# Performance work log

Measured on AMD Instinct MI355X. Metric: run time of the kernel, lower is better.

Reference implementation:

```python
import jax, jax.numpy as jnp
import numpy as np

B, N, D = 32, 2048, 320

def _init(key, shape, fan_in):
    return jax.random.normal(key, shape, dtype=jnp.float32) / np.sqrt(fan_in).astype(np.float32)

def setup_inputs() -> dict:
    key = jax.random.key(0)
    ks = jax.random.split(key, 11)
    return {
        "x": jax.random.normal(ks[0], (B, N, D), dtype=jnp.float32),
        # downs MLP: 320->160->80
        "W1": _init(ks[1], (320, 160), 320), "b1": jnp.zeros((160,), jnp.float32),
        "W2": _init(ks[2], (160, 80), 160),  "b2": jnp.zeros((80,), jnp.float32),
        # GraphConv1d layers: 80->40, 40->5
        "Wg1": _init(ks[3], (80, 40), 80),   "bg1": jnp.zeros((40,), jnp.float32),
        "Wg2": _init(ks[4], (40, 5), 40),    "bg2": jnp.zeros((5,), jnp.float32),
        # final classifier: 5->2
        "Wf": _init(ks[5], (5, 2), 5),       "bf": jnp.zeros((2,), jnp.float32),
    }

def _euclidean_adj(h):
    # h: [B, N, C] -> row-softmax of negative squared pairwise Euclidean distance [B, N, N]
    sq = jnp.sum(h * h, axis=-1, keepdims=True)               # [B, N, 1]
    d2 = sq - 2.0 * jnp.einsum('bnc,bmc->bnm', h, h) + jnp.swapaxes(sq, -1, -2)
    return jax.nn.softmax(-d2, axis=-1)

def _graph_conv(h, W, b):
    a = _euclidean_adj(h)                                     # dynamic adjacency
    agg = jnp.einsum('bnm,bmc->bnc', a, h)                    # neighbor aggregation
    return jax.nn.relu(agg @ W + b)

def reference(x, W1, b1, W2, b2, Wg1, bg1, Wg2, bg2, Wf, bf):
    h = jax.nn.relu(x @ W1 + b1)          # [B, N, 160]
    h = jax.nn.relu(h @ W2 + b2)          # [B, N, 80]
    h = _graph_conv(h, Wg1, bg1)          # [B, N, 40]
    h = _graph_conv(h, Wg2, bg2)          # [B, N, 5]
    h = jnp.mean(h, axis=1)               # Mean() over nodes -> [B, 5]
    logits = h @ Wf + bf                  # [B, 2]
    return jax.nn.softmax(logits, axis=-1)
```

## Files before the change

kernel.cpp:

```cpp
#include <hip/hip_runtime.h>
#include <math.h>

#define BB 32
#define NN 2048
#define D_IN 320
#define H1 160
#define H2 80
#define H4 5

typedef __attribute__((ext_vector_type(8))) short short8;
typedef __attribute__((ext_vector_type(4))) short short4v;
typedef __attribute__((ext_vector_type(4))) float f32x4;
typedef __attribute__((ext_vector_type(16))) float f32x16;

__device__ inline ushort f2bf(float f) {
    union { float f; unsigned u; } v; v.f = f;
    unsigned r = v.u + 0x7fff + ((v.u >> 16) & 1);
    return (ushort)(r >> 16);
}
__device__ inline float bf2f(ushort u) {
    union { float f; unsigned u; } v; v.u = ((unsigned)u) << 16;
    return v.f;
}
__device__ inline unsigned pkbf(float hi, float lo) {
    union { float f; unsigned u; } a, b; a.f = hi; b.f = lo;
    return __builtin_amdgcn_perm(a.u + 0x8000u, b.u + 0x8000u, 0x07060302u);
}
__device__ inline float fexp2(float x) {
    float r;
    asm("v_exp_f32 %0, %1" : "=v"(r) : "v"(x));
    return r;
}
union U2S { unsigned u[2]; short4v s; };
union U4S { unsigned u[4]; short8 s; short4v h[2]; };

#define LOG2E  1.44269504088896340736f
#define TWOL2E 2.88539008177792681472f

__global__ __launch_bounds__(256) void prep_weights_kernel(
    const float* __restrict__ W1, const float* __restrict__ W2,
    const float* __restrict__ Wg1, const float* __restrict__ bg1,
    const float* __restrict__ Wg2, const float* __restrict__ bg2,
    ushort* __restrict__ Wt1, ushort* __restrict__ Wt2,
    ushort* __restrict__ Wg1B, float* __restrict__ bg1P,
    ushort* __restrict__ Wg2A, float* __restrict__ bg2P)
{
    const int id0 = blockIdx.x * 256 + threadIdx.x;
    const int stride = gridDim.x * 256;
    for (int i = id0; i < H1 * D_IN; i += stride) {
        const int j = i / D_IN, c = i % D_IN;
        Wt1[i] = f2bf(W1[c * H1 + j]);
    }
    for (int i = id0; i < H2 * H1; i += stride) {
        const int j = i / H1, c = i % H1;
        Wt2[i] = f2bf(W2[c * H2 + j]);
    }
    for (int i = id0; i < 48 * 96; i += stride) {
        const int j = i / 96, c = i % 96;
        Wg1B[i] = (j < 40 && c < 80) ? f2bf(Wg1[c * 40 + j]) : (ushort)0;
    }
    for (int i = id0; i < 32 * 48; i += stride) {
        const int j = i / 48, c = i % 48;
        const int c4 = c & 15;
        const int pos = (c & ~15) + (c4 & 3) + (((c4 >> 3) & 1) << 2) + (((c4 >> 2) & 1) << 3);
        Wg2A[j * 48 + pos] = (j < 5 && c < 40) ? f2bf(Wg2[c * 5 + j]) : (ushort)0;
    }
    if (id0 < 64) bg1P[id0] = (id0 < 40) ? bg1[id0] : 0.f;
    if (id0 < 32) bg2P[id0] = (id0 < 5) ? bg2[id0] : 0.f;
}

__global__ __launch_bounds__(256) void mlp_mfma_kernel(
    const float* __restrict__ x,
    const ushort* __restrict__ Wt1, const float* __restrict__ b1,
    const ushort* __restrict__ Wt2, const float* __restrict__ b2,
    const ushort* __restrict__ Wg1B,
    ushort* __restrict__ h2, ushort* __restrict__ V1T, float* __restrict__ sq2)
{
    constexpr int XST  = 72;
    constexpr int W1ST = 72;
    constexpr int H1ST = 168;
    constexpr int RST  = 104;

    __shared__ __attribute__((aligned(16))) ushort h1t[64 * H1ST];
    __shared__ __attribute__((aligned(16))) ushort ws1[H1 * W1ST];
    __shared__ float b1s[H1];
    __shared__ float b2s[H2];

    ushort* xs = h1t;

    const int t = threadIdx.x;
    const int lane = t & 63, w = t >> 6;
    const int colid = lane & 15, quad = lane >> 4;
    const int i = blockIdx.x;
    const int b = ((i & 7) << 2) + ((i >> 3) & 3);
    const int n0 = (i >> 5) * 64;
    const int row0 = b * NN + n0;

    if (t < H1) b1s[t] = b1[t];
    if (t < H2) b2s[t] = b2[t];

    f32x4 c1[10];
    #pragma unroll
    for (int ns = 0; ns < 10; ++ns) c1[ns] = (f32x4){0.f, 0.f, 0.f, 0.f};

    float4 xr[4];
    short8 wr[5];
    {
        #pragma unroll
        for (int i2 = 0; i2 < 4; ++i2) {
            const int id = t + i2 * 256, row = id >> 4, c4 = id & 15;
            xr[i2] = *(const float4*)&x[(size_t)(row0 + row) * D_IN + c4 * 4];
        }
        #pragma unroll
        for (int i2 = 0; i2 < 5; ++i2) {
            const int id = t + i2 * 256, j = id >> 3, part = id & 7;
            wr[i2] = *(const short8*)&Wt1[j * D_IN + part * 8];
        }
    }

    for (int kc = 0; kc < 5; ++kc) {
        if (kc) __syncthreads();
        #pragma unroll
        for (int i2 = 0; i2 < 4; ++i2) {
            const int id = t + i2 * 256, row = id >> 4, c4 = id & 15;
            uint2 up;
            up.x = pkbf(xr[i2].y, xr[i2].x);
            up.y = pkbf(xr[i2].w, xr[i2].z);
            *(uint2*)&xs[row * XST + c4 * 4] = up;
        }
        #pragma unroll
        for (int i2 = 0; i2 < 5; ++i2) {
            const int id = t + i2 * 256, j = id >> 3, part = id & 7;
            *(short8*)&ws1[j * W1ST + part * 8] = wr[i2];
        }
        __syncthreads();
        if (kc < 4) {
            const int k0 = (kc + 1) * 64;
            #pragma unroll
            for (int i2 = 0; i2 < 4; ++i2) {
                const int id = t + i2 * 256, row = id >> 4, c4 = id & 15;
                xr[i2] = *(const float4*)&x[(size_t)(row0 + row) * D_IN + k0 + c4 * 4];
            }
            #pragma unroll
            for (int i2 = 0; i2 < 5; ++i2) {
                const int id = t + i2 * 256, j = id >> 3, part = id & 7;
                wr[i2] = *(const short8*)&Wt1[j * D_IN + k0 + part * 8];
            }
        }

        short8 af[2];
        #pragma unroll
        for (int kf = 0; kf < 2; ++kf)
            af[kf] = *(const short8*)&xs[(w * 16 + colid) * XST + kf * 32 + quad * 8];
        #pragma unroll
        for (int ns = 0; ns < 10; ++ns) {
            #pragma unroll
            for (int kf = 0; kf < 2; ++kf) {
                const short8 bf = *(const short8*)&ws1[(ns * 16 + colid) * W1ST + kf * 32 + quad * 8];
                c1[ns] = __builtin_amdgcn_mfma_f32_16x16x32_bf16(af[kf], bf, c1[ns], 0, 0, 0);
            }
        }
    }
    __syncthreads();

    #pragma unroll
    for (int ns = 0; ns < 10; ++ns) {
        const float bj = b1s[ns * 16 + colid];
        #pragma unroll
        for (int r = 0; r < 4; ++r)
            h1t[(w * 16 + quad * 4 + r) * H1ST + ns * 16 + colid] =
                f2bf(fmaxf(c1[ns][r] + bj, 0.f));
    }
    __asm__ volatile("s_waitcnt lgkmcnt(0)" ::: "memory");

    short8 a2[5];
    #pragma unroll
    for (int kf = 0; kf < 5; ++kf)
        a2[kf] = *(const short8*)&h1t[(w * 16 + colid) * H1ST + kf * 32 + quad * 8];

    f32x4 c2[5];
    #pragma unroll
    for (int js = 0; js < 5; ++js) {
        f32x4 acc = (f32x4){0.f, 0.f, 0.f, 0.f};
        #pragma unroll
        for (int kf = 0; kf < 5; ++kf) {
            const short8 wb = *(const short8*)&Wt2[(js * 16 + colid) * H1 + kf * 32 + quad * 8];
            acc = __builtin_amdgcn_mfma_f32_16x16x32_bf16(a2[kf], wb, acc, 0, 0, 0);
        }
        c2[js] = acc;
    }
    __syncthreads();

    ushort* h2row = h1t;
    float rsq[4] = {0.f, 0.f, 0.f, 0.f};
    #pragma unroll
    for (int js = 0; js < 5; ++js) {
        const float bj = b2s[js * 16 + colid];
        #pragma unroll
        for (int r = 0; r < 4; ++r) {
            const ushort u = f2bf(fmaxf(c2[js][r] + bj, 0.f));
            const float vv = bf2f(u);
            rsq[r] += vv * vv;
            h2[(size_t)(row0 + w * 16 + quad * 4 + r) * 80 + js * 16 + colid] = u;
            h2row[(w * 16 + quad * 4 + r) * RST + js * 16 + colid] = u;
        }
    }
    {
        const int zr = t >> 2, zc = t & 3;
        *(short4v*)&h2row[zr * RST + 80 + zc * 4] = (short4v){0, 0, 0, 0};
    }
    __asm__ volatile("s_waitcnt lgkmcnt(0)" ::: "memory");

    short8 a3[3];
    #pragma unroll
    for (int kf = 0; kf < 3; ++kf)
        a3[kf] = *(const short8*)&h2row[(w * 16 + colid) * RST + kf * 32 + quad * 8];

    f32x4 c3[3];
    #pragma unroll
    for (int js = 0; js < 3; ++js) {
        f32x4 acc = (f32x4){0.f, 0.f, 0.f, 0.f};
        #pragma unroll
        for (int kf = 0; kf < 3; ++kf) {
            const short8 wb = *(const short8*)&Wg1B[(js * 16 + colid) * 96 + kf * 32 + quad * 8];
            acc = __builtin_amdgcn_mfma_f32_16x16x32_bf16(a3[kf], wb, acc, 0, 0, 0);
        }
        c3[js] = acc;
    }

    #pragma unroll
    for (int m = 1; m <= 8; m <<= 1)
        #pragma unroll
        for (int r = 0; r < 4; ++r) rsq[r] += __shfl_xor(rsq[r], m);
    if (colid == 0) {
        #pragma unroll
        for (int r = 0; r < 4; ++r)
            sq2[(size_t)row0 + w * 16 + quad * 4 + r] = rsq[r] * LOG2E;
    }

    ushort* Tbuf = ws1;
    #pragma unroll
    for (int js = 0; js < 3; ++js)
        #pragma unroll
        for (int r = 0; r < 4; ++r)
            Tbuf[(js * 16 + colid) * 72 + w * 16 + quad * 4 + r] = f2bf(c3[js][r]);
    __syncthreads();
    const short8 ones8 = {16256, 16256, 16256, 16256, 16256, 16256, 16256, 16256};
    for (int id = t; id < 48 * 8; id += 256) {
        const int row = id >> 3, part = id & 7;
        const short8 val = (row == 40) ? ones8 : *(const short8*)&Tbuf[row * 72 + part * 8];
        *(short8*)&V1T[((size_t)b * 48 + row) * NN + n0 + part * 8] = val;
    }
}

template<int CK, int CV, int CVS, int ONES_CH, bool HAS_OUT, bool DO_MEAN, int C_OUT>
__global__ __launch_bounds__(256, 2) void attn_conv_kernel(
    const ushort* __restrict__ h, const ushort* __restrict__ hT,
    const float* __restrict__ sqg,
    const ushort* __restrict__ WtP, const float* __restrict__ biasP,
    ushort* __restrict__ ho, ushort* __restrict__ hoT, float* __restrict__ sqo,
    float* __restrict__ mean_out)
{
    constexpr int CF   = CK / 16;
    constexpr int CSV  = CV / 32;
    constexpr int KST  = CK + 8;
    constexpr int VST  = 64 + 8;
    constexpr int KPR  = CK / 8;
    constexpr int KTOT = 64 * KPR;
    constexpr int NK   = (KTOT + 255) / 256;
    constexpr int NV   = (CV * 8) / 256;
    constexpr int TST  = 136;
    constexpr int CS1  = ONES_CH / 32;
    constexpr int R1   = ((ONES_CH % 32) / 8) * 4 + (ONES_CH & 3);
    constexpr int BUFN = 64 * KST + CV * VST;

    __shared__ __attribute__((aligned(16))) ushort ldsbuf[2][BUFN];
    __shared__ __attribute__((aligned(16))) float sqs[2][64];

    const int t = threadIdx.x;
    const int lane = t & 63, w = t >> 6;
    const int m32 = lane & 31, hl = lane >> 5;
    const int i = blockIdx.x;
    const int b = ((i & 7) << 2) + ((i >> 3) & 3);
    const int n0blk = (i >> 5) * 128;
    const int qrow = n0blk + w * 32 + m32;

    short8 qf[CF];
    {
        const ushort* qr = h + ((size_t)b * NN + qrow) * CK;
        #pragma unroll
        for (int c = 0; c < CF; ++c)
            qf[c] = *(const short8*)&qr[c * 16 + hl * 8];
    }
    const float nsqnQL = -sqg[(size_t)b * NN + qrow];

    f32x16 o[CSV];
    #pragma unroll
    for (int cs = 0; cs < CSV; ++cs)
        #pragma unroll
        for (int r = 0; r < 16; ++r) o[cs][r] = 0.f;

    short8 kreg[NK], vreg[NV];
    float sqreg = 0.f;

    auto loadTile = [&](int n1) {
        const ushort* hsrc = h + ((size_t)b * NN + n1) * CK;
        #pragma unroll
        for (int i2 = 0; i2 < NK; ++i2) {
            const int id = t + i2 * 256;
            if (KTOT % 256 == 0 || id < KTOT)
                kreg[i2] = *(const short8*)&hsrc[id * 8];
        }
        #pragma unroll
        for (int i2 = 0; i2 < NV; ++i2) {
            const int id = t + i2 * 256, c = id >> 3, pt = id & 7;
            vreg[i2] = (c < CVS)
                ? *(const short8*)&hT[((size_t)b * CVS + c) * NN + n1 + pt * 8]
                : (short8){0, 0, 0, 0, 0, 0, 0, 0};
        }
        if (t < 64) sqreg = sqg[(size_t)b * NN + n1 + t];
    };
    auto stageTile = [&](int buf) {
        ushort* Kd = ldsbuf[buf];
        ushort* Vd = ldsbuf[buf] + 64 * KST;
        #pragma unroll
        for (int i2 = 0; i2 < NK; ++i2) {
            const int id = t + i2 * 256;
            if (KTOT % 256 == 0 || id < KTOT) {
                const int row = id / KPR, pt = id % KPR;
                *(short8*)&Kd[row * KST + pt * 8] = kreg[i2];
            }
        }
        #pragma unroll
        for (int i2 = 0; i2 < NV; ++i2) {
            const int id = t + i2 * 256, c = id >> 3, pt = id & 7;
            const int colb = ((pt >> 1) << 4) + ((pt & 1) << 2);
            U4S vv; vv.s = vreg[i2];
            *(short4v*)&Vd[c * VST + colb]     = vv.h[0];
            *(short4v*)&Vd[c * VST + colb + 8] = vv.h[1];
        }
        if (t < 64) sqs[buf][t] = sqreg;
    };

    loadTile(0);
    stageTile(0);
    __syncthreads();
    loadTile(64);

    for (int it = 0; it < NN / 64; ++it) {
        const int cur = it & 1;
        const ushort* Krow = ldsbuf[cur];
        const ushort* Vcol = ldsbuf[cur] + 64 * KST;

        short8 kf_[2][CF];
        short8 vf_[2][2][CSV];
        f32x4  smv_[2][4];
        #pragma unroll
        for (int T = 0; T < 2; ++T) {
            #pragma unroll
            for (int c = 0; c < CF; ++c)
                kf_[T][c] = *(const short8*)&Krow[(T * 32 + m32) * KST + c * 16 + hl * 8];
            #pragma unroll
            for (int c = 0; c < 2; ++c)
                #pragma unroll
                for (int cs = 0; cs < CSV; ++cs)
                    vf_[T][c][cs] = *(const short8*)&Vcol[(cs * 32 + m32) * VST + (T * 2 + c) * 16 + hl * 8];
            #pragma unroll
            for (int g = 0; g < 4; ++g)
                smv_[T][g] = *(const f32x4*)&sqs[cur][T * 32 + g * 8 + hl * 4];
        }

        if (it + 1 < NN / 64) {
            stageTile(cur ^ 1);
            if (it + 2 < NN / 64) loadTile((it + 2) * 64);
        }

        f32x16 st0, st1;
        #pragma unroll
        for (int r = 0; r < 16; ++r) { st0[r] = 0.f; st1[r] = 0.f; }
        #pragma unroll
        for (int c = 0; c < CF; ++c) {
            st0 = __builtin_amdgcn_mfma_f32_32x32x16_bf16(kf_[0][c], qf[c], st0, 0, 0, 0);
            st1 = __builtin_amdgcn_mfma_f32_32x32x16_bf16(kf_[1][c], qf[c], st1, 0, 0, 0);
        }

        #pragma unroll
        for (int T = 0; T < 2; ++T) {
            const f32x16& st = T ? st1 : st0;
            float p[16];
            #pragma unroll
            for (int g = 0; g < 4; ++g) {
                #pragma unroll
                for (int r2 = 0; r2 < 4; ++r2)
                    p[g * 4 + r2] = fexp2(fmaf(st[g * 4 + r2], TWOL2E,
                                               nsqnQL - smv_[T][g][r2]));
            }
            #pragma unroll
            for (int c = 0; c < 2; ++c) {
                U4S pk_;
                #pragma unroll
                for (int bq = 0; bq < 4; ++bq)
                    pk_.u[bq] = pkbf(p[c * 8 + bq * 2 + 1], p[c * 8 + bq * 2]);
                #pragma unroll
                for (int cs = 0; cs < CSV; ++cs)
                    o[cs] = __builtin_amdgcn_mfma_f32_32x32x16_bf16(vf_[T][c][cs], pk_.s, o[cs], 0, 0, 0);
            }
        }
        __syncthreads();
    }

    float rsv = (hl == 0) ? o[CS1][R1] : 0.f;
    rsv += __shfl_xor(rsv, 32);
    const float rinv = 1.f / rsv;

    if constexpr (DO_MEAN) {
        float msum[4];
        #pragma unroll
        for (int r2 = 0; r2 < 4; ++r2)
            msum[r2] = fmaxf(o[0][r2] * rinv + biasP[hl * 4 + r2], 0.f);
        #pragma unroll
        for (int s = 1; s <= 16; s <<= 1)
            #pragma unroll
            for (int r2 = 0; r2 < 4; ++r2) msum[r2] += __shfl_xor(msum[r2], s);
        if (m32 == 0) {
            if (hl == 0) {
                #pragma unroll
                for (int r2 = 0; r2 < 4; ++r2)
                    atomicAdd(&mean_out[b * C_OUT + r2], msum[r2] * (1.f / NN));
            } else {
                atomicAdd(&mean_out[b * C_OUT + 4], msum[0] * (1.f / NN));
            }
        }
    }

    if constexpr (HAS_OUT) {
        float vv[CSV][16];
        float rsq = 0.f;
        #pragma unroll
        for (int cs = 0; cs < CSV; ++cs) {
            #pragma unroll
            for (int g = 0; g < 4; ++g) {
                const int jb = cs * 32 + g * 8 + hl * 4;
                const f32x4 bv = *(const f32x4*)&biasP[jb];
                float v[4];
                #pragma unroll
                for (int r2 = 0; r2 < 4; ++r2) {
                    float val = fmaxf(o[cs][g * 4 + r2] * rinv + bv[r2], 0.f);
                    if (cs == CS1 && g * 4 + r2 == R1) val = 0.f;
                    v[r2] = val;
                    rsq += val * val;
                    vv[cs][g * 4 + r2] = val;
                }
                if (jb < 48) {
                    U2S uo;
                    uo.u[0] = pkbf(v[1], v[0]);
                    uo.u[1] = pkbf(v[3], v[2]);
                    *(short4v*)&ho[((size_t)b * NN + qrow) * 48 + jb] = uo.s;
                }
            }
        }
        const float rsq2 = rsq + __shfl_xor(rsq, 32);
        if (hl == 0) sqo[(size_t)b * NN + qrow] = rsq2 * LOG2E;

        short8 ob2[3];
        #pragma unroll
        for (int cc = 0; cc < 3; ++cc) {
            const int cs = cc >> 1, c2 = cc & 1;
            U4S ob_;
            #pragma unroll
            for (int bq = 0; bq < 4; ++bq)
                ob_.u[bq] = pkbf(vv[cs][c2 * 8 + bq * 2 + 1], vv[cs][c2 * 8 + bq * 2]);
            ob2[cc] = ob_.s;
        }
        f32x16 acc;
        #pragma unroll
        for (int r = 0; r < 16; ++r) acc[r] = 0.f;
        #pragma unroll
        for (int cc = 0; cc < 3; ++cc) {
            const short8 wa = *(const short8*)&WtP[(size_t)m32 * 48 + cc * 16 + hl * 8];
            acc = __builtin_amdgcn_mfma_f32_32x32x16_bf16(wa, ob2[cc], acc, 0, 0, 0);
        }

        ushort* Tbuf = (ushort*)ldsbuf;
        #pragma unroll
        for (int g = 0; g < 2; ++g)
            #pragma unroll
            for (int r2 = 0; r2 < 4; ++r2)
                Tbuf[(g * 8 + hl * 4 + r2) * TST + w * 32 + m32] = f2bf(acc[g * 4 + r2]);
        __syncthreads();
        const short8 ones8 = {16256, 16256, 16256, 16256, 16256, 16256, 16256, 16256};
        {
            const int row = t >> 4, part = t & 15;
            const short8 val = (row == 8) ? ones8
                             : *(const short8*)&Tbuf[row * TST + part * 8];
            *(short8*)&hoT[((size_t)b * 16 + row) * NN + n0blk + part * 8] = val;
        }
    }
}

__global__ __launch_bounds__(64) void final_kernel(
    const float* __restrict__ mean, const float* __restrict__ Wf,
    const float* __restrict__ bf, float* __restrict__ out)
{
    const int t = threadIdx.x;
    const int b = t >> 1, k = t & 1;
    float acc = bf[k];
    #pragma unroll
    for (int c = 0; c < H4; ++c) acc += mean[b * H4 + c] * Wf[c * 2 + k];
    const float other = __shfl_xor(acc, 1);
    const float mx = fmaxf(acc, other);
    const float e  = __expf(acc - mx);
    const float eo = __expf(other - mx);
    out[t] = e / (e + eo);
}

extern "C" void kernel_launch(void* const* d_in, const int* in_sizes, int n_in,
                              void* d_out, int out_size, void* d_ws, size_t ws_size,
                              hipStream_t stream) {
    const float* x   = (const float*)d_in[0];
    const float* W1  = (const float*)d_in[1];
    const float* b1  = (const float*)d_in[2];
    const float* W2  = (const float*)d_in[3];
    const float* b2  = (const float*)d_in[4];
    const float* Wg1 = (const float*)d_in[5];
    const float* bg1 = (const float*)d_in[6];
    const float* Wg2 = (const float*)d_in[7];
    const float* bg2 = (const float*)d_in[8];
    const float* Wf  = (const float*)d_in[9];
    const float* bf  = (const float*)d_in[10];

    ushort* h2   = (ushort*)d_ws;
    ushort* V1T  = h2  + (size_t)BB * NN * 80;
    float*  sq2  = (float*)(V1T + (size_t)BB * 48 * NN);
    ushort* h3   = (ushort*)(sq2 + (size_t)BB * NN);
    ushort* V2T  = h3  + (size_t)BB * NN * 48;
    float*  sq3  = (float*)(V2T + (size_t)BB * 16 * NN);
    float*  meanb = sq3 + (size_t)BB * NN;
    ushort* Wt1  = (ushort*)(meanb + 160);
    ushort* Wt2  = Wt1 + (size_t)H1 * D_IN;
    ushort* Wg1B = Wt2 + (size_t)H2 * H1;
    float*  bg1P = (float*)(Wg1B + 48 * 96);
    ushort* Wg2A = (ushort*)(bg1P + 64);
    float*  bg2P = (float*)(Wg2A + 32 * 48);

    hipMemsetAsync(meanb, 0, BB * H4 * sizeof(float), stream);

    prep_weights_kernel<<<64, 256, 0, stream>>>(W1, W2, Wg1, bg1, Wg2, bg2,
                                                Wt1, Wt2, Wg1B, bg1P, Wg2A, bg2P);
    mlp_mfma_kernel<<<BB * NN / 64, 256, 0, stream>>>(x, Wt1, b1, Wt2, b2, Wg1B,
                                                      h2, V1T, sq2);
    attn_conv_kernel<80, 64, 48, 40, true,  false, 0><<<BB * NN / 128, 256, 0, stream>>>(
        h2, V1T, sq2, Wg2A, bg1P, h3, V2T, sq3, nullptr);
    attn_conv_kernel<48, 32, 16, 8,  false, true,  5><<<BB * NN / 128, 256, 0, stream>>>(
        h3, V2T, sq3, nullptr, bg2P, nullptr, nullptr, nullptr, meanb);
    final_kernel<<<1, 64, 0, stream>>>(meanb, Wf, bf, (float*)d_out);
}
```

Measured before the change: 258.4 us.

## Software-pipeline QK MFMA with previous tile's exp and PV in graph attention

```diff
diff --git a/kernel.cpp b/kernel.cpp
--- a/kernel.cpp
+++ b/kernel.cpp
@@ -235,7 +235,7 @@
     if (colid == 0) {
         #pragma unroll
         for (int r = 0; r < 4; ++r)
-            sq2[(size_t)row0 + w * 16 + quad * 4 + r] = rsq[r] * LOG2E;
+            sq2[(size_t)row0 + w * 16 + quad * 4 + r] = rsq[r] * 0.5f;
     }
 
     ushort* Tbuf = ws1;
@@ -273,6 +273,7 @@
     constexpr int CS1  = ONES_CH / 32;
     constexpr int R1   = ((ONES_CH % 32) / 8) * 4 + (ONES_CH & 3);
     constexpr int BUFN = 64 * KST + CV * VST;
+    constexpr int NIT  = NN / 64;
 
     __shared__ __attribute__((aligned(16))) ushort ldsbuf[2][BUFN];
     __shared__ __attribute__((aligned(16))) float sqs[2][64];
@@ -292,7 +293,7 @@
         for (int c = 0; c < CF; ++c)
             qf[c] = *(const short8*)&qr[c * 16 + hl * 8];
     }
-    const float nsqnQL = -sqg[(size_t)b * NN + qrow];
+    const float nsqn = -sqg[(size_t)b * NN + qrow];
 
     f32x16 o[CSV];
     #pragma unroll
@@ -342,59 +343,51 @@
         if (t < 64) sqs[buf][t] = sqreg;
     };
 
-    loadTile(0);
-    stageTile(0);
-    __syncthreads();
-    loadTile(64);
-
-    for (int it = 0; it < NN / 64; ++it) {
-        const int cur = it & 1;
-        const ushort* Krow = ldsbuf[cur];
-        const ushort* Vcol = ldsbuf[cur] + 64 * KST;
-
-        short8 kf_[2][CF];
-        short8 vf_[2][2][CSV];
-        f32x4  smv_[2][4];
-        #pragma unroll
-        for (int T = 0; T < 2; ++T) {
+    auto preloadK = [&](const ushort* Krow, short8 (&kf)[2][CF]) {
+        #pragma unroll
+        for (int T = 0; T < 2; ++T)
             #pragma unroll
             for (int c = 0; c < CF; ++c)
-                kf_[T][c] = *(const short8*)&Krow[(T * 32 + m32) * KST + c * 16 + hl * 8];
+                kf[T][c] = *(const short8*)&Krow[(T * 32 + m32) * KST + c * 16 + hl * 8];
+    };
+    auto initST = [&](int cur, f32x16& s0, f32x16& s1) {
+        #pragma unroll
+        for (int g = 0; g < 4; ++g) {
+            const f32x4 sm0 = *(const f32x4*)&sqs[cur][g * 8 + hl * 4];
+            const f32x4 sm1 = *(const f32x4*)&sqs[cur][32 + g * 8 + hl * 4];
+            #pragma unroll
+            for (int r2 = 0; r2 < 4; ++r2) {
+                s0[g * 4 + r2] = nsqn - sm0[r2];
+                s1[g * 4 + r2] = nsqn - sm1[r2];
+            }
+        }
+    };
+    auto smfma = [&](short8 (&kf)[2][CF], f32x16& s0, f32x16& s1) {
+        #pragma unroll
+        for (int c = 0; c < CF; ++c) {
+            s0 = __builtin_amdgcn_mfma_f32_32x32x16_bf16(kf[0][c], qf[c], s0, 0, 0, 0);
+            s1 = __builtin_amdgcn_mfma_f32_32x32x16_bf16(kf[1][c], qf[c], s1, 0, 0, 0);
+        }
+    };
+    auto preloadV = [&](const ushort* Vcol, short8 (&vf)[2][2][CSV]) {
+        #pragma unroll
+        for (int T = 0; T < 2; ++T)
             #pragma unroll
             for (int c = 0; c < 2; ++c)
                 #pragma unroll
                 for (int cs = 0; cs < CSV; ++cs)
-                    vf_[T][c][cs] = *(const short8*)&Vcol[(cs * 32 + m32) * VST + (T * 2 + c) * 16 + hl * 8];
+                    vf[T][c][cs] = *(const short8*)&Vcol[(cs * 32 + m32) * VST + (T * 2 + c) * 16 + hl * 8];
+    };
+    auto expPV = [&](const f32x16& s0, const f32x16& s1, const short8 (&vf)[2][2][CSV]) {
+        #pragma unroll
+        for (int T = 0; T < 2; ++T) {
+            const f32x16& st = T ? s1 : s0;
+            float p[16];
             #pragma unroll
             for (int g = 0; g < 4; ++g)
-                smv_[T][g] = *(const f32x4*)&sqs[cur][T * 32 + g * 8 + hl * 4];
-        }
-
-        if (it + 1 < NN / 64) {
-            stageTile(cur ^ 1);
-            if (it + 2 < NN / 64) loadTile((it + 2) * 64);
-        }
-
-        f32x16 st0, st1;
-        #pragma unroll
-        for (int r = 0; r < 16; ++r) { st0[r] = 0.f; st1[r] = 0.f; }
-        #pragma unroll
-        for (int c = 0; c < CF; ++c) {
-            st0 = __builtin_amdgcn_mfma_f32_32x32x16_bf16(kf_[0][c], qf[c], st0, 0, 0, 0);
-            st1 = __builtin_amdgcn_mfma_f32_32x32x16_bf16(kf_[1][c], qf[c], st1, 0, 0, 0);
-        }
-
-        #pragma unroll
-        for (int T = 0; T < 2; ++T) {
-            const f32x16& st = T ? st1 : st0;
-            float p[16];
-            #pragma unroll
-            for (int g = 0; g < 4; ++g) {
                 #pragma unroll
                 for (int r2 = 0; r2 < 4; ++r2)
-                    p[g * 4 + r2] = fexp2(fmaf(st[g * 4 + r2], TWOL2E,
-                                               nsqnQL - smv_[T][g][r2]));
-            }
+                    p[g * 4 + r2] = fexp2(st[g * 4 + r2] * TWOL2E);
             #pragma unroll
             for (int c = 0; c < 2; ++c) {
                 U4S pk_;
@@ -403,11 +396,66 @@
                     pk_.u[bq] = pkbf(p[c * 8 + bq * 2 + 1], p[c * 8 + bq * 2]);
                 #pragma unroll
                 for (int cs = 0; cs < CSV; ++cs)
-                    o[cs] = __builtin_amdgcn_mfma_f32_32x32x16_bf16(vf_[T][c][cs], pk_.s, o[cs], 0, 0, 0);
-            }
-        }
+                    o[cs] = __builtin_amdgcn_mfma_f32_32x32x16_bf16(vf[T][c][cs], pk_.s, o[cs], 0, 0, 0);
+            }
+        }
+    };
+
+    loadTile(0);
+    stageTile(0);
+    __syncthreads();
+    loadTile(64);
+
+    f32x16 stA0, stA1, stB0, stB1;
+    short8 vfA[2][2][CSV], vfB[2][2][CSV];
+
+    {
+        short8 kf[2][CF];
+        preloadK(ldsbuf[0], kf);
+        initST(0, stA0, stA1);
+        preloadV(ldsbuf[0] + 64 * KST, vfA);
+        stageTile(1);
+        loadTile(128);
+        smfma(kf, stA0, stA1);
         __syncthreads();
     }
+
+    #pragma unroll 1
+    for (int k = 0; k < NIT / 2 - 1; ++k) {
+        {
+            short8 kf[2][CF];
+            preloadK(ldsbuf[1], kf);
+            initST(1, stB0, stB1);
+            stageTile(0);
+            loadTile((3 + 2 * k) * 64);
+            smfma(kf, stB0, stB1);
+            preloadV(ldsbuf[1] + 64 * KST, vfB);
+            expPV(stA0, stA1, vfA);
+            __syncthreads();
+        }
+        {
+            short8 kf[2][CF];
+            preloadK(ldsbuf[0], kf);
+            initST(0, stA0, stA1);
+            stageTile(1);
+            if (k < NIT / 2 - 2) loadTile((4 + 2 * k) * 64);
+            smfma(kf, stA0, stA1);
+            preloadV(ldsbuf[0] + 64 * KST, vfA);
+            expPV(stB0, stB1, vfB);
+            __syncthreads();
+        }
+    }
+
+    {
+        short8 kf[2][CF];
+        preloadK(ldsbuf[1], kf);
+        initST(1, stB0, stB1);
+        smfma(kf, stB0, stB1);
+        preloadV(ldsbuf[1] + 64 * KST, vfB);
+        expPV(stA0, stA1, vfA);
+        __syncthreads();
+    }
+    expPV(stB0, stB1, vfB);
 
     float rsv = (hl == 0) ? o[CS1][R1] : 0.f;
     rsv += __shfl_xor(rsv, 32);
@@ -448,7 +496,6 @@
                     float val = fmaxf(o[cs][g * 4 + r2] * rinv + bv[r2], 0.f);
                     if (cs == CS1 && g * 4 + r2 == R1) val = 0.f;
                     v[r2] = val;
-                    rsq += val * val;
                     vv[cs][g * 4 + r2] = val;
                 }
                 if (jb < 48) {
@@ -456,11 +503,16 @@
                     uo.u[0] = pkbf(v[1], v[0]);
                     uo.u[1] = pkbf(v[3], v[2]);
                     *(short4v*)&ho[((size_t)b * NN + qrow) * 48 + jb] = uo.s;
+                    #pragma unroll
+                    for (int r2 = 0; r2 < 4; ++r2) {
+                        const float vs = bf2f((ushort)(uo.u[r2 >> 1] >> ((r2 & 1) * 16)));
+                        rsq += vs * vs;
+                    }
                 }
             }
         }
         const float rsq2 = rsq + __shfl_xor(rsq, 32);
-        if (hl == 0) sqo[(size_t)b * NN + qrow] = rsq2 * LOG2E;
+        if (hl == 0) sqo[(size_t)b * NN + qrow] = rsq2 * 0.5f;
 
         short8 ob2[3];
         #pragma unroll
```

Measured after the change: 259.7 us. Within noise of the previous version (+0.5%).
